# Performance work log

Measured on AMD Instinct MI355X. Metric: run time of the kernel, lower is better.

The kernel has to match this reference:

```python
import jax, jax.numpy as jnp
import numpy as np
from jax import lax

B_, L_, D_MODEL, D_FF = 8, 1024, 512, 2048
D_STATE, D_CONV, EXPAND = 16, 4, 2
D_IN = EXPAND * D_MODEL
DT_RANK = (D_MODEL + 15) // 16  # 32


def _ln(x, g, b, eps=1e-5):
    m = jnp.mean(x, -1, keepdims=True)
    v = jnp.var(x, -1, keepdims=True)
    return (x - m) / jnp.sqrt(v + eps) * g + b


def _selective_scan(u, dt, A, Bm, Cm, D):
    # u, dt: (B,L,d_in); Bm, Cm: (B,L,d_state); A: (d_in,d_state); D: (d_in,)
    def step(h, xs):
        dt_t, B_t, C_t, u_t = xs  # (B,d_in),(B,ds),(B,ds),(B,d_in)
        dA = jnp.exp(dt_t[..., None] * A)                       # (B,d_in,ds)
        h = dA * h + (dt_t * u_t)[..., None] * B_t[:, None, :]  # (B,d_in,ds)
        y = jnp.einsum('bds,bs->bd', h, C_t)
        return h, y

    h0 = jnp.zeros((u.shape[0], D_IN, D_STATE), u.dtype)
    xs = (dt.transpose(1, 0, 2), Bm.transpose(1, 0, 2),
          Cm.transpose(1, 0, 2), u.transpose(1, 0, 2))
    _, ys = lax.scan(step, h0, xs)           # (L,B,d_in)
    return ys.transpose(1, 0, 2) + u * D


def _mamba(x, in_w, conv_w, conv_b, xp_w, dtp_w, dtp_b, A_log, D, out_w):
    xz = x @ in_w.T                              # (B,L,2*d_in)
    xs, z = jnp.split(xz, 2, axis=-1)
    # causal depthwise conv1d over L
    xc = lax.conv_general_dilated(xs.transpose(0, 2, 1), conv_w, (1,),
                                  [(D_CONV - 1, 0)], feature_group_count=D_IN)
    xc = jax.nn.silu(xc + conv_b[None, :, None]).transpose(0, 2, 1)  # (B,L,d_in)
    x_dbl = xc @ xp_w.T
    dt, Bm, Cm = jnp.split(x_dbl, [DT_RANK, DT_RANK + D_STATE], axis=-1)
    dt = jax.nn.softplus(dt @ dtp_w.T + dtp_b)
    A = -jnp.exp(A_log)
    y = _selective_scan(xc, dt, A, Bm, Cm, D)
    y = y * jax.nn.silu(z)
    return y @ out_w.T


def _forward(x,
             in1_w, conv1d1_w, conv1d1_b, xp1_w, dtp1_w, dtp1_b, Alog1, D1, outp1_w,
             in2_w, conv1d2_w, conv1d2_b, xp2_w, dtp2_w, dtp2_b, Alog2, D2, outp2_w,
             c1_w, c1_b, c2_w, c2_b, ln1_g, ln1_b, ln2_g, ln2_b):
    x_res = x  # dropout is identity in eval
    fwd = _mamba(x, in1_w, conv1d1_w, conv1d1_b, xp1_w, dtp1_w, dtp1_b, Alog1, D1, outp1_w)
    bwd = _mamba(jnp.flip(x, 1), in2_w, conv1d2_w, conv1d2_b, xp2_w, dtp2_w, dtp2_b,
                 Alog2, D2, outp2_w)
    new_x = fwd + jnp.flip(bwd, 1)
    x = _ln(new_x + x_res, ln1_g, ln1_b)
    y = jax.nn.gelu(jnp.einsum('bld,fd->blf', x, c1_w[:, :, 0]) + c1_b, approximate=False)
    y = jnp.einsum('blf,df->bld', y, c2_w[:, :, 0]) + c2_b
    return _ln(x + y, ln2_g, ln2_b)


def setup_inputs() -> dict:
    key = jax.random.key(0)
    ks = iter(jax.random.split(key, 32))
    rn = lambda shape, s=0.02: jax.random.normal(next(ks), shape, jnp.float32) * s

    def mamba_params():
        return dict(in_w=rn((2 * D_IN, D_MODEL)), conv_w=rn((D_IN, 1, D_CONV)),
                    conv_b=rn((D_IN,)), xp_w=rn((DT_RANK + 2 * D_STATE, D_IN)),
                    dtp_w=rn((D_IN, DT_RANK)), dtp_b=rn((D_IN,)),
                    A_log=jnp.log(jnp.tile(jnp.arange(1., D_STATE + 1.), (D_IN, 1))).astype(jnp.float32),
                    D=jnp.ones((D_IN,), jnp.float32), out_w=rn((D_MODEL, D_IN)))

    m1, m2 = mamba_params(), mamba_params()
    return {
        'x': jax.random.normal(next(ks), (B_, L_, D_MODEL), jnp.float32),
        'in1_w': m1['in_w'], 'conv1d1_w': m1['conv_w'], 'conv1d1_b': m1['conv_b'],
        'xp1_w': m1['xp_w'], 'dtp1_w': m1['dtp_w'], 'dtp1_b': m1['dtp_b'],
        'Alog1': m1['A_log'], 'D1': m1['D'], 'outp1_w': m1['out_w'],
        'in2_w': m2['in_w'], 'conv1d2_w': m2['conv_w'], 'conv1d2_b': m2['conv_b'],
        'xp2_w': m2['xp_w'], 'dtp2_w': m2['dtp_w'], 'dtp2_b': m2['dtp_b'],
        'Alog2': m2['A_log'], 'D2': m2['D'], 'outp2_w': m2['out_w'],
        'c1_w': rn((D_FF, D_MODEL, 1)), 'c1_b': rn((D_FF,)),
        'c2_w': rn((D_MODEL, D_FF, 1)), 'c2_b': rn((D_MODEL,)),
        'ln1_g': jnp.ones((D_MODEL,), jnp.float32), 'ln1_b': jnp.zeros((D_MODEL,), jnp.float32),
        'ln2_g': jnp.ones((D_MODEL,), jnp.float32), 'ln2_b': jnp.zeros((D_MODEL,), jnp.float32),
    }


def reference(x,
              in1_w, conv1d1_w, conv1d1_b, xp1_w, dtp1_w, dtp1_b, Alog1, D1, outp1_w,
              in2_w, conv1d2_w, conv1d2_b, xp2_w, dtp2_w, dtp2_b, Alog2, D2, outp2_w,
              c1_w, c1_b, c2_w, c2_b, ln1_g, ln1_b, ln2_g, ln2_b):
    return _forward(x,
                    in1_w, conv1d1_w, conv1d1_b, xp1_w, dtp1_w, dtp1_b, Alog1, D1, outp1_w,
                    in2_w, conv1d2_w, conv1d2_b, xp2_w, dtp2_w, dtp2_b, Alog2, D2, outp2_w,
                    c1_w, c1_b, c2_w, c2_b, ln1_g, ln1_b, ln2_g, ln2_b)
```

## Files before the change

kernel.cpp:

```cpp
#include <hip/hip_runtime.h>
#include <hip/hip_bf16.h>
#include <math.h>

#define B_SZ 8
#define L_SZ 1024
#define DM 512
#define DFF 2048
#define DIN 1024
#define DSTATE 16
#define DTRANK 32
#define MROWS (B_SZ * L_SZ)
#define CH 256
#define NCH 4

typedef __hip_bfloat16 bf16;
typedef unsigned short u16;
using f32x4 = __attribute__((ext_vector_type(4))) float;
using bfrag = __attribute__((ext_vector_type(8))) short;

__device__ inline float ldf(const float* p, long i) { return p[i]; }
__device__ inline float ldf(const bf16* p, long i) {
  return __uint_as_float((unsigned)((const u16*)p)[i] << 16);
}
__device__ inline void stf(float* p, long i, float v) { p[i] = v; }
__device__ inline void stf(bf16* p, long i, float v) { p[i] = __float2bfloat16(v); }
__device__ inline float b2f(u16 x) {
  return __uint_as_float((unsigned)x << 16);
}
__device__ inline u16 f2b(float v) {
  union { bf16 h; u16 u; } c;
  c.h = __float2bfloat16(v);
  return c.u;
}

__device__ inline float fexp2(float x) {
  float r;
  asm("v_exp_f32 %0, %1" : "=v"(r) : "v"(x));
  return r;
}

typedef __attribute__((address_space(1))) const void g_void;
typedef __attribute__((address_space(3))) void l_void;
__device__ inline void gl_lds16(const void* g, void* l) {
  __builtin_amdgcn_global_load_lds((g_void*)g, (l_void*)l, 16, 0, 0);
}

__device__ inline float4 ld4f_bt(const float* p) { return *(const float4*)p; }
__device__ inline float4 ld4f_bt(const bf16* p) {
  ushort4 u = *(const ushort4*)p;
  float4 v;
  v.x = b2f(u.x); v.y = b2f(u.y); v.z = b2f(u.z); v.w = b2f(u.w);
  return v;
}

__device__ inline void ld16f(const float* p, uint4& lo, uint4& hi) {
  float4 a = *(const float4*)p, b = *(const float4*)(p + 4);
  float4 c = *(const float4*)(p + 8), d = *(const float4*)(p + 12);
  union { uint4 v; u16 s[8]; } L, H;
  L.s[0] = f2b(a.x); L.s[1] = f2b(a.y); L.s[2] = f2b(a.z); L.s[3] = f2b(a.w);
  L.s[4] = f2b(b.x); L.s[5] = f2b(b.y); L.s[6] = f2b(b.z); L.s[7] = f2b(b.w);
  H.s[0] = f2b(c.x); H.s[1] = f2b(c.y); H.s[2] = f2b(c.z); H.s[3] = f2b(c.w);
  H.s[4] = f2b(d.x); H.s[5] = f2b(d.y); H.s[6] = f2b(d.z); H.s[7] = f2b(d.w);
  lo = L.v; hi = H.v;
}

__device__ inline float dpp_add_r8(float x) {
  float r; asm("v_add_f32 %0, %1, %2 row_ror:8" : "=v"(r) : "v"(x), "v"(x)); return r;
}
__device__ inline float dpp_add_r4(float x) {
  float r; asm("v_add_f32 %0, %1, %2 row_ror:4" : "=v"(r) : "v"(x), "v"(x)); return r;
}
__device__ inline float dpp_add_r2(float x) {
  float r; asm("v_add_f32 %0, %1, %2 row_ror:2" : "=v"(r) : "v"(x), "v"(x)); return r;
}
__device__ inline float dpp_add_r1(float x) {
  float r; asm("v_add_f32 %0, %1, %2 row_ror:1" : "=v"(r) : "v"(x), "v"(x)); return r;
}
__device__ inline float row16_sum(float x) {
  return dpp_add_r1(dpp_add_r2(dpp_add_r4(dpp_add_r8(x))));
}

__device__ inline int flipL(int r) {
  int t = r & (L_SZ - 1);
  return (r - t) + (L_SZ - 1 - t);
}

__global__ __launch_bounds__(256) void cvt8_k(
    const float* s0, const float* s1, const float* s2, const float* s3,
    const float* s4, const float* s5, const float* s6, const float* s7,
    bf16* d0, bf16* d1, bf16* d2, bf16* d3,
    bf16* d4, bf16* d5, bf16* d6, bf16* d7) {
  int blk = blockIdx.x;
  const float* s; bf16* d; long off;
  if (blk < 2048)       { s = s0; d = d0; off = (long)blk * 256; }
  else if (blk < 4096)  { s = s1; d = d1; off = (long)(blk - 2048) * 256; }
  else if (blk < 6144)  { s = s2; d = d2; off = (long)(blk - 4096) * 256; }
  else if (blk < 8192)  { s = s3; d = d3; off = (long)(blk - 6144) * 256; }
  else if (blk < 10240) { s = s4; d = d4; off = (long)(blk - 8192) * 256; }
  else if (blk < 12288) { s = s5; d = d5; off = (long)(blk - 10240) * 256; }
  else if (blk < 16384) { s = s6; d = d6; off = (long)(blk - 12288) * 256; }
  else                  { s = s7; d = d7; off = (long)(blk - 16384) * 256; }
  off += threadIdx.x;
  d[off] = __float2bfloat16(s[off]);
}

constexpr int MEPI_STORE2 = 0;
constexpr int MEPI_GATE2 = 1;
constexpr int MEPI_BIAS_GELU = 2;
constexpr int MEPI_BIAS_RES = 3;

template <int EPI, typename TA, typename TO>
__global__ __launch_bounds__(256) void mgemm_k(
    const TA* __restrict__ Ab, int lda,
    const bf16* __restrict__ Wb, int ldw,
    TO* __restrict__ C, TO* __restrict__ C2, int ldc,
    const float* __restrict__ bias,
    const float* __restrict__ res,
    int K) {
  constexpr bool ABF = (sizeof(TA) == 2);
  __shared__ u16 Wsm[128][32];
  __shared__ u16 AsmL[ABF ? 128 : 1][32];
  __shared__ u16 AsmP[ABF ? 1 : 128][ABF ? 1 : 40];
  const int tid = threadIdx.x;
  const int m0 = blockIdx.y * 128;
  const int n0 = blockIdx.x * 128;

  const int srow4 = tid >> 2;
  const int q16 = tid & 3;
  const u16* Wg0 = (const u16*)Wb + (long)(n0 + srow4) * ldw + q16 * 8;
  const u16* Wg1 = (const u16*)Wb + (long)(n0 + 64 + srow4) * ldw + q16 * 8;
  char* WsmB = (char*)&Wsm[0][0] + (tid >> 6) * 1024;

  const u16* Ag0 = (const u16*)Ab + (long)(m0 + srow4) * lda + q16 * 8;
  const u16* Ag1 = (const u16*)Ab + (long)(m0 + 64 + srow4) * lda + q16 * 8;
  char* AsmB = (char*)&AsmL[0][0] + (tid >> 6) * 1024;

  const int srow = tid >> 1;
  const int scol = (tid & 1) * 16;
  const TA* Agf = Ab + (long)(m0 + srow) * lda + scol;

  const int lane = tid & 63, quad = lane >> 4, l16 = lane & 15;
  const int wid = tid >> 6;
  const int wm = (wid & 1) * 64, wn = (wid >> 1) * 64;

  f32x4 acc[4][4];
#pragma unroll
  for (int i = 0; i < 4; ++i)
#pragma unroll
    for (int j = 0; j < 4; ++j) acc[i][j] = {0.f, 0.f, 0.f, 0.f};

  for (int k0 = 0; k0 < K; k0 += 32) {
    uint4 av0, av1;
    if constexpr (!ABF) ld16f((const float*)(Agf + k0), av0, av1);
    __syncthreads();
    gl_lds16(Wg0 + k0, WsmB);
    gl_lds16(Wg1 + k0, WsmB + 4096);
    if constexpr (ABF) {
      gl_lds16(Ag0 + k0, AsmB);
      gl_lds16(Ag1 + k0, AsmB + 4096);
    } else {
      *(uint4*)&AsmP[srow][scol] = av0;
      *(uint4*)&AsmP[srow][scol + 8] = av1;
    }
    __syncthreads();
    bfrag a[4], b[4];
#pragma unroll
    for (int mi = 0; mi < 4; ++mi) {
      if constexpr (ABF)
        a[mi] = *(const bfrag*)&AsmL[wm + mi * 16 + l16][quad * 8];
      else
        a[mi] = *(const bfrag*)&AsmP[wm + mi * 16 + l16][quad * 8];
    }
#pragma unroll
    for (int ni = 0; ni < 4; ++ni)
      b[ni] = *(const bfrag*)&Wsm[wn + ni * 16 + l16][quad * 8];
#pragma unroll
    for (int mi = 0; mi < 4; ++mi)
#pragma unroll
      for (int ni = 0; ni < 4; ++ni)
        acc[mi][ni] = __builtin_amdgcn_mfma_f32_16x16x32_bf16(
            a[mi], b[ni], acc[mi][ni], 0, 0, 0);
  }

  const bool second = (n0 >= DIN);
#pragma unroll
  for (int mi = 0; mi < 4; ++mi)
#pragma unroll
    for (int ni = 0; ni < 4; ++ni)
#pragma unroll
      for (int r = 0; r < 4; ++r) {
        int row = m0 + wm + mi * 16 + quad * 4 + r;
        int col = n0 + wn + ni * 16 + l16;
        float v = acc[mi][ni][r];
        if (EPI == MEPI_STORE2) {
          if (second) stf(C2, (long)flipL(row) * ldc + (col - DIN), v);
          else stf(C, (long)row * ldc + col, v);
        } else if (EPI == MEPI_GATE2) {
          TO* T = second ? C2 : C;
          long oi = second ? ((long)flipL(row) * ldc + (col - DIN))
                           : ((long)row * ldc + col);
          float y = ldf((const bf16*)T, oi);
          float sz = v / (1.f + __expf(-v));
          stf(T, oi, y * sz);
        } else if (EPI == MEPI_BIAS_GELU) {
          long oi = (long)row * ldc + col;
          v += bias[col];
          v = 0.5f * v * (1.f + erff(v * 0.70710678118654752440f));
          stf(C, oi, v);
        } else if (EPI == MEPI_BIAS_RES) {
          long oi = (long)row * ldc + col;
          ((float*)C)[oi] = v + bias[col] + res[oi];
        }
      }
}

__global__ __launch_bounds__(256) void mmerge_k(
    const bf16* __restrict__ y1, const bf16* __restrict__ y2,
    const bf16* __restrict__ W1, const bf16* __restrict__ W2,
    const float* __restrict__ xres, float* __restrict__ newx) {
  __shared__ u16 AsmL[128][32];
  __shared__ u16 Wsm[128][32];
  const int tid = threadIdx.x;
  const int m0 = blockIdx.y * 128;
  const int n0 = blockIdx.x * 128;

  const int srow4 = tid >> 2;
  const int q16 = tid & 3;
  int r1a = m0 + srow4, r1b = m0 + 64 + srow4;
  int r2a = flipL(r1a), r2b = flipL(r1b);
  const u16* A1g0 = (const u16*)y1 + (long)r1a * DIN + q16 * 8;
  const u16* A1g1 = (const u16*)y1 + (long)r1b * DIN + q16 * 8;
  const u16* A2g0 = (const u16*)y2 + (long)r2a * DIN + q16 * 8;
  const u16* A2g1 = (const u16*)y2 + (long)r2b * DIN + q16 * 8;
  const u16* W1g0 = (const u16*)W1 + (long)(n0 + srow4) * DIN + q16 * 8;
  const u16* W1g1 = (const u16*)W1 + (long)(n0 + 64 + srow4) * DIN + q16 * 8;
  const u16* W2g0 = (const u16*)W2 + (long)(n0 + srow4) * DIN + q16 * 8;
  const u16* W2g1 = (const u16*)W2 + (long)(n0 + 64 + srow4) * DIN + q16 * 8;
  char* AsmB = (char*)&AsmL[0][0] + (tid >> 6) * 1024;
  char* WsmB = (char*)&Wsm[0][0] + (tid >> 6) * 1024;

  const int lane = tid & 63, quad = lane >> 4, l16 = lane & 15;
  const int wid = tid >> 6;
  const int wm = (wid & 1) * 64, wn = (wid >> 1) * 64;

  f32x4 acc[4][4];
#pragma unroll
  for (int i = 0; i < 4; ++i)
#pragma unroll
    for (int j = 0; j < 4; ++j) acc[i][j] = {0.f, 0.f, 0.f, 0.f};

  for (int k0 = 0; k0 < 2 * DIN; k0 += 32) {
    const bool ph2 = (k0 >= DIN);
    const int kk = k0 & (DIN - 1);
    const u16* a0 = ph2 ? A2g0 : A1g0;
    const u16* a1 = ph2 ? A2g1 : A1g1;
    const u16* w0 = ph2 ? W2g0 : W1g0;
    const u16* w1 = ph2 ? W2g1 : W1g1;
    __syncthreads();
    gl_lds16(a0 + kk, AsmB);
    gl_lds16(a1 + kk, AsmB + 4096);
    gl_lds16(w0 + kk, WsmB);
    gl_lds16(w1 + kk, WsmB + 4096);
    __syncthreads();
    bfrag a[4], b[4];
#pragma unroll
    for (int mi = 0; mi < 4; ++mi)
      a[mi] = *(const bfrag*)&AsmL[wm + mi * 16 + l16][quad * 8];
#pragma unroll
    for (int ni = 0; ni < 4; ++ni)
      b[ni] = *(const bfrag*)&Wsm[wn + ni * 16 + l16][quad * 8];
#pragma unroll
    for (int mi = 0; mi < 4; ++mi)
#pragma unroll
      for (int ni = 0; ni < 4; ++ni)
        acc[mi][ni] = __builtin_amdgcn_mfma_f32_16x16x32_bf16(
            a[mi], b[ni], acc[mi][ni], 0, 0, 0);
  }

#pragma unroll
  for (int mi = 0; mi < 4; ++mi)
#pragma unroll
    for (int ni = 0; ni < 4; ++ni)
#pragma unroll
      for (int r = 0; r < 4; ++r) {
        int row = m0 + wm + mi * 16 + quad * 4 + r;
        int col = n0 + wn + ni * 16 + l16;
        long oi = (long)row * DM + col;
        newx[oi] = acc[mi][ni][r] + xres[oi];
      }
}

constexpr int EPI_NONE = 0;
constexpr int EPI_SOFTPLUS_ROW = 1;

#define BM 64
#define BN 64
#define BKK 16

template <int EPI, typename TB, typename TO>
__global__ __launch_bounds__(256) void gemmBT_k(
    const float* __restrict__ A,
    const TB* __restrict__ B,
    TO* __restrict__ C, int N,
    const float* __restrict__ bias, int K) {
  __shared__ float As[BKK][BM + 4];
  __shared__ float Bs[BKK][BN + 4];
  const int tid = threadIdx.x;
  const int m0 = blockIdx.y * BM;
  const int n0 = blockIdx.x * BN;
  const int tx = tid & 15;
  const int ty = tid >> 4;
  const int lrow = tid >> 2;
  const int lcol = (tid & 3) * 4;
  const int kr = tid >> 4;
  const int nc = (tid & 15) * 4;

  const float* Arow = A + (long)(m0 + lrow) * K;

  float acc[4][4] = {};
  for (int k0 = 0; k0 < K; k0 += BKK) {
    float4 av = *(const float4*)(Arow + k0 + lcol);
    float4 bv = ld4f_bt(B + (long)(k0 + kr) * N + n0 + nc);
    As[lcol + 0][lrow] = av.x; As[lcol + 1][lrow] = av.y;
    As[lcol + 2][lrow] = av.z; As[lcol + 3][lrow] = av.w;
    Bs[kr][nc + 0] = bv.x; Bs[kr][nc + 1] = bv.y;
    Bs[kr][nc + 2] = bv.z; Bs[kr][nc + 3] = bv.w;
    __syncthreads();
#pragma unroll
    for (int k = 0; k < BKK; ++k) {
      float a[4], b[4];
#pragma unroll
      for (int i = 0; i < 4; ++i) a[i] = As[k][ty * 4 + i];
#pragma unroll
      for (int j = 0; j < 4; ++j) b[j] = Bs[k][tx * 4 + j];
#pragma unroll
      for (int i = 0; i < 4; ++i)
#pragma unroll
        for (int j = 0; j < 4; ++j) acc[i][j] += a[i] * b[j];
    }
    __syncthreads();
  }

#pragma unroll
  for (int i = 0; i < 4; ++i) {
    int r = m0 + ty * 4 + i;
#pragma unroll
    for (int j = 0; j < 4; ++j) {
      int c = n0 + tx * 4 + j;
      float v = acc[i][j];
      if (EPI == EPI_SOFTPLUS_ROW) {
        v += bias[r];
        v = (v > 20.f) ? v : log1pf(__expf(v));
      }
      stf(C, (long)r * N + c, v);
    }
  }
}

#define XSLICE 4
#define XSZ ((long)64 * MROWS)

__global__ __launch_bounds__(256) void xprojs_k(
    const float* __restrict__ A1, const bf16* __restrict__ B1,
    float* __restrict__ P1,
    const float* __restrict__ A2, const bf16* __restrict__ B2,
    float* __restrict__ P2) {
  __shared__ float As[BKK][BM + 4];
  __shared__ float Bs[BKK][BN + 4];
  const int tid = threadIdx.x;
  const int n0 = blockIdx.x * BN;
  const int slice = blockIdx.y;
  const int kbeg = slice * (DIN / XSLICE);
  const int dir = blockIdx.z;
  const float* A = dir ? A2 : A1;
  const bf16* Bm = dir ? B2 : B1;
  float* P = (dir ? P2 : P1) + (long)slice * XSZ;
  const int N = MROWS, K = DIN;
  const int tx = tid & 15;
  const int ty = tid >> 4;
  const int lrow = tid >> 2;
  const int lcol = (tid & 3) * 4;
  const int kr = tid >> 4;
  const int nc = (tid & 15) * 4;

  const float* Arow = A + (long)lrow * K;

  float acc[4][4] = {};
  for (int k0 = kbeg; k0 < kbeg + DIN / XSLICE; k0 += BKK) {
    float4 av = *(const float4*)(Arow + k0 + lcol);
    float4 bv = ld4f_bt(Bm + (long)(k0 + kr) * N + n0 + nc);
    As[lcol + 0][lrow] = av.x; As[lcol + 1][lrow] = av.y;
    As[lcol + 2][lrow] = av.z; As[lcol + 3][lrow] = av.w;
    Bs[kr][nc + 0] = bv.x; Bs[kr][nc + 1] = bv.y;
    Bs[kr][nc + 2] = bv.z; Bs[kr][nc + 3] = bv.w;
    __syncthreads();
#pragma unroll
    for (int k = 0; k < BKK; ++k) {
      float a[4], b[4];
#pragma unroll
      for (int i = 0; i < 4; ++i) a[i] = As[k][ty * 4 + i];
#pragma unroll
      for (int j = 0; j < 4; ++j) b[j] = Bs[k][tx * 4 + j];
#pragma unroll
      for (int i = 0; i < 4; ++i)
#pragma unroll
        for (int j = 0; j < 4; ++j) acc[i][j] += a[i] * b[j];
    }
    __syncthreads();
  }

#pragma unroll
  for (int i = 0; i < 4; ++i) {
    int r = ty * 4 + i;
#pragma unroll
    for (int j = 0; j < 4; ++j) {
      int c = n0 + tx * 4 + j;
      P[(long)r * N + c] = acc[i][j];
    }
  }
}

__global__ __launch_bounds__(256) void xred_k(
    const float* __restrict__ P1, float* __restrict__ o1,
    const float* __restrict__ P2, float* __restrict__ o2) {
  long i = (long)blockIdx.x * 256 + threadIdx.x;
  const float* P = blockIdx.y ? P2 : P1;
  float* o = blockIdx.y ? o2 : o1;
  o[i] = P[i] + P[i + XSZ] + P[i + 2 * XSZ] + P[i + 3 * XSZ];
}

__global__ __launch_bounds__(256) void convT_k(
    const bf16* __restrict__ xs, const float* __restrict__ w,
    const float* __restrict__ b, bf16* __restrict__ xcT) {
  __shared__ u16 T[64][72];
  int c0 = blockIdx.x * 64;
  int r0 = blockIdx.y * 64;
  int tid = threadIdx.x;
  int tr = tid >> 2;
  int tc = (tid & 3) * 16;

  const u16* src = (const u16*)xs + (long)(r0 + tr) * DIN + c0 + tc;
  uint4 v0 = *(const uint4*)src;
  uint4 v1 = *(const uint4*)(src + 8);
  u16 tmp[16];
  *(uint4*)tmp = v0;
  *(uint4*)(tmp + 8) = v1;
#pragma unroll
  for (int j = 0; j < 16; ++j) T[tc + j][tr + 3] = tmp[j];
  bool head = (r0 & (L_SZ - 1)) == 0;
  if (tid < 12) {
    int hr = tid >> 2;
    int seg = (tid & 3) * 16;
    if (head) {
#pragma unroll
      for (int j = 0; j < 16; ++j) T[seg + j][hr] = 0;
    } else {
      const u16* hs = (const u16*)xs + (long)(r0 - 3 + hr) * DIN + c0 + seg;
      uint4 h0 = *(const uint4*)hs;
      uint4 h1 = *(const uint4*)(hs + 8);
      u16 ht[16];
      *(uint4*)ht = h0;
      *(uint4*)(ht + 8) = h1;
#pragma unroll
      for (int j = 0; j < 16; ++j) T[seg + j][hr] = ht[j];
    }
  }
  __syncthreads();

  int d = c0 + tr;
  float w0 = w[d * 4 + 0], w1 = w[d * 4 + 1], w2 = w[d * 4 + 2], w3 = w[d * 4 + 3];
  float bd = b[d];
  float X[19];
#pragma unroll
  for (int k = 0; k < 19; ++k) X[k] = b2f(T[tr][tc + k]);
  u16 o[16];
#pragma unroll
  for (int j = 0; j < 16; ++j) {
    float acc = bd + w0 * X[j] + w1 * X[j + 1] + w2 * X[j + 2] + w3 * X[j + 3];
    o[j] = f2b(acc / (1.f + __expf(-acc)));
  }
  u16* dst = (u16*)xcT + (long)d * MROWS + r0 + tc;
  *(uint4*)dst = *(uint4*)o;
  *(uint4*)(dst + 8) = *(uint4*)(o + 8);
}

__global__ __launch_bounds__(256, 4) void scan1_k(
    const u16* __restrict__ dtT1, const u16* __restrict__ dtT2,
    const u16* __restrict__ uT1, const u16* __restrict__ uT2,
    const float* __restrict__ xd1, const float* __restrict__ xd2,
    const float* __restrict__ Alog1, const float* __restrict__ Alog2,
    bf16* __restrict__ hl1, bf16* __restrict__ hl2,
    float* __restrict__ sd1, float* __restrict__ sd2) {
  int blk = blockIdx.x;
  int dblk = blk & 15;
  int r = blk >> 4;
  int c = r % 3; r /= 3;
  int b = r & 7;
  int dir = r >> 3;
  int tid = threadIdx.x;
  int s = tid & 15;
  int gi = tid >> 4;
  int d0 = dblk * 64 + gi * 4;
  const u16* dtT = dir ? dtT2 : dtT1;
  const u16* uT = dir ? uT2 : uT1;
  const float* xd = dir ? xd2 : xd1;
  const float* Alog = dir ? Alog2 : Alog1;
  bf16* hl = dir ? hl2 : hl1;
  float* sd = dir ? sd2 : sd1;

  float A2[4], h[4], sdt[4];
#pragma unroll
  for (int dd = 0; dd < 4; ++dd) {
    A2[dd] = -__expf(Alog[(d0 + dd) * DSTATE + s]) * 1.4426950408889634f;
    h[dd] = 0.f;
    sdt[dd] = 0.f;
  }
  long t0 = (long)b * L_SZ + c * CH;
  const u16* pdt = dtT + (long)d0 * MROWS + t0;
  const u16* pu = uT + (long)d0 * MROWS + t0;
  const float* pB = xd + (long)(DTRANK + s) * MROWS + t0;

  for (int g = 0; g < CH / 8; ++g) {
    union { uint4 v; u16 a[8]; } dt8[4], u8[4];
    union { float4 v[2]; float a[8]; } B8;
#pragma unroll
    for (int dd = 0; dd < 4; ++dd) {
      dt8[dd].v = *(const uint4*)(pdt + (long)dd * MROWS + g * 8);
      u8[dd].v = *(const uint4*)(pu + (long)dd * MROWS + g * 8);
    }
    B8.v[0] = *(const float4*)(pB + g * 8);
    B8.v[1] = *(const float4*)(pB + g * 8 + 4);
#pragma unroll
    for (int j = 0; j < 8; ++j) {
      float Bj = B8.a[j];
#pragma unroll
      for (int dd = 0; dd < 4; ++dd) {
        float dtv = b2f(dt8[dd].a[j]);
        float uv = b2f(u8[dd].a[j]);
        float da = fexp2(dtv * A2[dd]);
        h[dd] = da * h[dd] + (dtv * uv) * Bj;
        sdt[dd] += dtv;
      }
    }
  }
#pragma unroll
  for (int dd = 0; dd < 4; ++dd) {
    int ci = (b * 3 + c) * 1024 + d0 + dd;
    hl[(long)ci * 16 + s] = __float2bfloat16(h[dd]);
    if (s == 0) sd[ci] = sdt[dd];
  }
}

__global__ __launch_bounds__(256, 4) void scan2_k(
    const u16* __restrict__ dtT1, const u16* __restrict__ dtT2,
    const u16* __restrict__ uT1, const u16* __restrict__ uT2,
    const float* __restrict__ xd1, const float* __restrict__ xd2,
    const float* __restrict__ Alog1, const float* __restrict__ Alog2,
    const float* __restrict__ D1, const float* __restrict__ D2,
    const bf16* __restrict__ hl1, const bf16* __restrict__ hl2,
    const float* __restrict__ sd1, const float* __restrict__ sd2,
    bf16* __restrict__ y1, bf16* __restrict__ y2) {
  int blk = blockIdx.x;
  int dblk = blk & 15;
  int c = (blk >> 4) & 3;
  int b = (blk >> 6) & 7;
  int dir = blk >> 9;
  int tid = threadIdx.x;
  int s = tid & 15;
  int gi = tid >> 4;
  int d0 = dblk * 64 + gi * 4;
  const u16* dtT = dir ? dtT2 : dtT1;
  const u16* uT = dir ? uT2 : uT1;
  const float* xd = dir ? xd2 : xd1;
  const float* Alog = dir ? Alog2 : Alog1;
  const float* Dp = dir ? D2 : D1;
  const bf16* hl = dir ? hl2 : hl1;
  const float* sd = dir ? sd2 : sd1;
  bf16* out = dir ? y2 : y1;

  float A2[4], h[4], Dd[4];
#pragma unroll
  for (int dd = 0; dd < 4; ++dd) {
    A2[dd] = -__expf(Alog[(d0 + dd) * DSTATE + s]) * 1.4426950408889634f;
    Dd[dd] = Dp[d0 + dd];
    h[dd] = 0.f;
  }

  for (int cc = 0; cc < c; ++cc) {
#pragma unroll
    for (int dd = 0; dd < 4; ++dd) {
      int ci = (b * 3 + cc) * 1024 + d0 + dd;
      float P = fexp2(A2[dd] * sd[ci]);
      h[dd] = h[dd] * P + b2f(((const u16*)hl)[(long)ci * 16 + s]);
    }
  }

  long t0 = (long)b * L_SZ + c * CH;
  const u16* pdt = dtT + (long)d0 * MROWS + t0;
  const u16* pu = uT + (long)d0 * MROWS + t0;
  const float* pB = xd + (long)(DTRANK + s) * MROWS + t0;
  const float* pC = xd + (long)(DTRANK + DSTATE + s) * MROWS + t0;
  u16* outb = (u16*)out + (long)b * L_SZ * DIN + (long)c * CH * DIN + d0;

  for (int g = 0; g < CH / 8; ++g) {
    union { uint4 v; u16 a[8]; } dt8[4], u8[4];
    union { float4 v[2]; float a[8]; } B8, C8;
#pragma unroll
    for (int dd = 0; dd < 4; ++dd) {
      dt8[dd].v = *(const uint4*)(pdt + (long)dd * MROWS + g * 8);
      u8[dd].v = *(const uint4*)(pu + (long)dd * MROWS + g * 8);
    }
    B8.v[0] = *(const float4*)(pB + g * 8);
    B8.v[1] = *(const float4*)(pB + g * 8 + 4);
    C8.v[0] = *(const float4*)(pC + g * 8);
    C8.v[1] = *(const float4*)(pC + g * 8 + 4);
    u16* og = outb + (long)g * 8 * DIN;
#pragma unroll
    for (int j = 0; j < 8; ++j) {
      float Bj = B8.a[j];
      float Cj = C8.a[j];
      u16 o4[4];
#pragma unroll
      for (int dd = 0; dd < 4; ++dd) {
        float dtv = b2f(dt8[dd].a[j]);
        float uv = b2f(u8[dd].a[j]);
        float da = fexp2(dtv * A2[dd]);
        h[dd] = da * h[dd] + (dtv * uv) * Bj;
        float q = row16_sum(h[dd] * Cj);
        o4[dd] = f2b(q + Dd[dd] * uv);
      }
      if (s == 0) *(uint2*)(og + (long)j * DIN) = *(uint2*)o4;
    }
  }
}

__global__ __launch_bounds__(256) void ln_k(
    const float* __restrict__ xin, const float* __restrict__ g,
    const float* __restrict__ bb, float* __restrict__ out,
    bf16* __restrict__ outb) {
  int row = blockIdx.x;
  const float* p = xin + (long)row * DM;
  int tid = threadIdx.x;
  float x0 = p[tid], x1 = p[tid + 256];
  float sum = x0 + x1;
  float sq = x0 * x0 + x1 * x1;
#pragma unroll
  for (int o = 1; o < 64; o <<= 1) {
    sum += __shfl_xor(sum, o, 64);
    sq += __shfl_xor(sq, o, 64);
  }
  __shared__ float ssum[4], ssq[4];
  int wv = tid >> 6;
  if ((tid & 63) == 0) { ssum[wv] = sum; ssq[wv] = sq; }
  __syncthreads();
  sum = ssum[0] + ssum[1] + ssum[2] + ssum[3];
  sq = ssq[0] + ssq[1] + ssq[2] + ssq[3];
  float mean = sum * (1.f / DM);
  float var = sq * (1.f / DM) - mean * mean;
  float rstd = rsqrtf(var + 1e-5f);
  float v0 = (x0 - mean) * rstd * g[tid] + bb[tid];
  float v1 = (x1 - mean) * rstd * g[tid + 256] + bb[tid + 256];
  out[(long)row * DM + tid] = v0;
  out[(long)row * DM + tid + 256] = v1;
  if (outb) {
    stf(outb, (long)row * DM + tid, v0);
    stf(outb, (long)row * DM + tid + 256, v1);
  }
}

extern "C" void kernel_launch(void* const* d_in, const int* in_sizes, int n_in,
                              void* d_out, int out_size, void* d_ws, size_t ws_size,
                              hipStream_t stream) {
  const float* x = (const float*)d_in[0];
  const float* in1_w = (const float*)d_in[1];
  const float* conv1_w = (const float*)d_in[2];
  const float* conv1_b = (const float*)d_in[3];
  const float* xp1_w = (const float*)d_in[4];
  const float* dtp1_w = (const float*)d_in[5];
  const float* dtp1_b = (const float*)d_in[6];
  const float* Alog1 = (const float*)d_in[7];
  const float* D1 = (const float*)d_in[8];
  const float* outp1_w = (const float*)d_in[9];
  const float* in2_w = (const float*)d_in[10];
  const float* conv2_w = (const float*)d_in[11];
  const float* conv2_b = (const float*)d_in[12];
  const float* xp2_w = (const float*)d_in[13];
  const float* dtp2_w = (const float*)d_in[14];
  const float* dtp2_b = (const float*)d_in[15];
  const float* Alog2 = (const float*)d_in[16];
  const float* D2 = (const float*)d_in[17];
  const float* outp2_w = (const float*)d_in[18];
  const float* c1_w = (const float*)d_in[19];
  const float* c1_b = (const float*)d_in[20];
  const float* c2_w = (const float*)d_in[21];
  const float* c2_b = (const float*)d_in[22];
  const float* ln1_g = (const float*)d_in[23];
  const float* ln1_b = (const float*)d_in[24];
  const float* ln2_g = (const float*)d_in[25];
  const float* ln2_b = (const float*)d_in[26];

  const long MB = 1024L * 1024;
  char* wsb = (char*)d_ws;
  bf16* A = (bf16*)(wsb + 0 * MB);
  bf16* B = (bf16*)(wsb + 16 * MB);
  bf16* C = (bf16*)(wsb + 32 * MB);
  bf16* D = (bf16*)(wsb + 48 * MB);
  bf16* E = (bf16*)(wsb + 64 * MB);
  bf16* F = (bf16*)(wsb + 80 * MB);
  float* Bf = (float*)B;
  float* Cf = (float*)C;
  float* Af = (float*)A;
  bf16* ffn = C;
  float* P1 = (float*)A;
  float* P2 = (float*)D;

  char* ob = (char*)d_out;
  bf16* Wxs = (bf16*)(ob + 0 * MB);
  bf16* Wg = (bf16*)(ob + 2 * MB);
  bf16* o1b = (bf16*)(ob + 4 * MB);
  bf16* o2b = (bf16*)(ob + 5 * MB);
  bf16* c1b = (bf16*)(ob + 6 * MB);
  bf16* c2b = (bf16*)(ob + 8 * MB);
  float* xdT1 = (float*)(ob + 10 * MB);
  float* xdT2 = (float*)(ob + 12 * MB);
  float* sd1 = (float*)(ob + 14 * MB);
  float* sd2 = (float*)(ob + 14 * MB + 131072);
  bf16* hl1 = (bf16*)(ob + 14 * MB + 262144);
  bf16* hl2 = (bf16*)(ob + 15 * MB);

  const long HWN = (long)DIN * DM;

  dim3 blk(256);
  dim3 gP2(2 * DIN / 128, MROWS / 128);
  dim3 gM(DM / 128, MROWS / 128);
  dim3 gF(DFF / 128, MROWS / 128);
  dim3 gC(DIN / 64, MROWS / 64);
  dim3 gXs(MROWS / BN, XSLICE, 2);
  dim3 gXr(XSZ / 256, 2);
  dim3 gD(MROWS / BN, DIN / BM);

  cvt8_k<<<20480, blk, 0, stream>>>(
      in1_w, in2_w, in1_w + HWN, in2_w + HWN, outp1_w, outp2_w, c1_w, c2_w,
      Wxs, Wxs + HWN, Wg, Wg + HWN, o1b, o2b, c1b, c2b);

  mgemm_k<MEPI_STORE2, float, bf16><<<gP2, blk, 0, stream>>>(
      x, DM, Wxs, DM, A, D, DIN, nullptr, nullptr, DM);

  convT_k<<<gC, blk, 0, stream>>>(A, conv1_w, conv1_b, B);
  convT_k<<<gC, blk, 0, stream>>>(D, conv2_w, conv2_b, E);

  xprojs_k<<<gXs, blk, 0, stream>>>(xp1_w, B, P1, xp2_w, E, P2);
  xred_k<<<gXr, blk, 0, stream>>>(P1, xdT1, P2, xdT2);

  gemmBT_k<EPI_SOFTPLUS_ROW, float, bf16><<<gD, blk, 0, stream>>>(
      dtp1_w, xdT1, C, MROWS, dtp1_b, DTRANK);
  gemmBT_k<EPI_SOFTPLUS_ROW, float, bf16><<<gD, blk, 0, stream>>>(
      dtp2_w, xdT2, F, MROWS, dtp2_b, DTRANK);

  scan1_k<<<2 * 8 * 3 * 16, blk, 0, stream>>>(
      (const u16*)C, (const u16*)F, (const u16*)B, (const u16*)E,
      xdT1, xdT2, Alog1, Alog2, hl1, hl2, sd1, sd2);
  scan2_k<<<2 * 8 * 4 * 16, blk, 0, stream>>>(
      (const u16*)C, (const u16*)F, (const u16*)B, (const u16*)E,
      xdT1, xdT2, Alog1, Alog2, D1, D2, hl1, hl2, sd1, sd2, A, D);

  mgemm_k<MEPI_GATE2, float, bf16><<<gP2, blk, 0, stream>>>(
      x, DM, Wg, DM, A, D, DIN, nullptr, nullptr, DM);

  mmerge_k<<<gM, blk, 0, stream>>>(A, D, o1b, o2b, x, Cf);

  ln_k<<<MROWS, blk, 0, stream>>>(Cf, ln1_g, ln1_b, Bf, E);

  mgemm_k<MEPI_BIAS_GELU, bf16, bf16><<<gF, blk, 0, stream>>>(
      E, DM, c1b, DM, ffn, nullptr, DFF, c1_b, nullptr, DM);
  mgemm_k<MEPI_BIAS_RES, bf16, float><<<gM, blk, 0, stream>>>(
      ffn, DFF, c2b, DFF, Af, nullptr, DM, c2_b, Bf, DFF);

  ln_k<<<MROWS, blk, 0, stream>>>(Af, ln2_g, ln2_b, (float*)d_out, nullptr);
}
```

Before: 726.5 us.

## Pre-convert x to bf16, shrink N=512 GEMM tiles, batch both directions per launch

Converts the fp32 input x to bf16 up front, adding it to the weight-conversion kernel and a separate conversion before the gate GEMM, so the in-projection GEMMs can stream A via global_load_lds instead of converting on load. The out-projection merge and FFN second GEMM (N=512) switch from 128x128 tiles to 64x64 tiles, giving more blocks on the GPU for these narrow outputs. The conv and dt-projection kernels now handle both directions in one launch via blockIdx.z. These changes add extra conversion passes over x and smaller tiles with less reuse per block, in exchange for fewer launches and better occupancy.

After: 765.0 us. 5.3% more time.

```diff
diff --git a/kernel.cpp b/kernel.cpp
--- a/kernel.cpp
+++ b/kernel.cpp
@@ -53,17 +53,6 @@
   return v;
 }
 
-__device__ inline void ld16f(const float* p, uint4& lo, uint4& hi) {
-  float4 a = *(const float4*)p, b = *(const float4*)(p + 4);
-  float4 c = *(const float4*)(p + 8), d = *(const float4*)(p + 12);
-  union { uint4 v; u16 s[8]; } L, H;
-  L.s[0] = f2b(a.x); L.s[1] = f2b(a.y); L.s[2] = f2b(a.z); L.s[3] = f2b(a.w);
-  L.s[4] = f2b(b.x); L.s[5] = f2b(b.y); L.s[6] = f2b(b.z); L.s[7] = f2b(b.w);
-  H.s[0] = f2b(c.x); H.s[1] = f2b(c.y); H.s[2] = f2b(c.z); H.s[3] = f2b(c.w);
-  H.s[4] = f2b(d.x); H.s[5] = f2b(d.y); H.s[6] = f2b(d.z); H.s[7] = f2b(d.w);
-  lo = L.v; hi = H.v;
-}
-
 __device__ inline float dpp_add_r8(float x) {
   float r; asm("v_add_f32 %0, %1, %2 row_ror:8" : "=v"(r) : "v"(x), "v"(x)); return r;
 }
@@ -85,11 +74,18 @@
   return (r - t) + (L_SZ - 1 - t);
 }
 
-__global__ __launch_bounds__(256) void cvt8_k(
+__global__ __launch_bounds__(256) void cvt_k(const float* __restrict__ s,
+                                             bf16* __restrict__ d, int n) {
+  int i = blockIdx.x * 256 + threadIdx.x;
+  if (i < n) d[i] = __float2bfloat16(s[i]);
+}
+
+__global__ __launch_bounds__(256) void cvt9_k(
     const float* s0, const float* s1, const float* s2, const float* s3,
     const float* s4, const float* s5, const float* s6, const float* s7,
+    const float* s8,
     bf16* d0, bf16* d1, bf16* d2, bf16* d3,
-    bf16* d4, bf16* d5, bf16* d6, bf16* d7) {
+    bf16* d4, bf16* d5, bf16* d6, bf16* d7, bf16* d8) {
   int blk = blockIdx.x;
   const float* s; bf16* d; long off;
   if (blk < 2048)       { s = s0; d = d0; off = (long)blk * 256; }
@@ -99,7 +95,8 @@
   else if (blk < 10240) { s = s4; d = d4; off = (long)(blk - 8192) * 256; }
   else if (blk < 12288) { s = s5; d = d5; off = (long)(blk - 10240) * 256; }
   else if (blk < 16384) { s = s6; d = d6; off = (long)(blk - 12288) * 256; }
-  else                  { s = s7; d = d7; off = (long)(blk - 16384) * 256; }
+  else if (blk < 20480) { s = s7; d = d7; off = (long)(blk - 16384) * 256; }
+  else                  { s = s8; d = d8; off = (long)(blk - 20480) * 256; }
   off += threadIdx.x;
   d[off] = __float2bfloat16(s[off]);
 }
@@ -107,20 +104,16 @@
 constexpr int MEPI_STORE2 = 0;
 constexpr int MEPI_GATE2 = 1;
 constexpr int MEPI_BIAS_GELU = 2;
-constexpr int MEPI_BIAS_RES = 3;
-
-template <int EPI, typename TA, typename TO>
+
+template <int EPI, typename TO>
 __global__ __launch_bounds__(256) void mgemm_k(
-    const TA* __restrict__ Ab, int lda,
+    const bf16* __restrict__ Ab, int lda,
     const bf16* __restrict__ Wb, int ldw,
     TO* __restrict__ C, TO* __restrict__ C2, int ldc,
     const float* __restrict__ bias,
-    const float* __restrict__ res,
     int K) {
-  constexpr bool ABF = (sizeof(TA) == 2);
   __shared__ u16 Wsm[128][32];
-  __shared__ u16 AsmL[ABF ? 128 : 1][32];
-  __shared__ u16 AsmP[ABF ? 1 : 128][ABF ? 1 : 40];
+  __shared__ u16 AsmL[128][32];
   const int tid = threadIdx.x;
   const int m0 = blockIdx.y * 128;
   const int n0 = blockIdx.x * 128;
@@ -135,10 +128,6 @@
   const u16* Ag1 = (const u16*)Ab + (long)(m0 + 64 + srow4) * lda + q16 * 8;
   char* AsmB = (char*)&AsmL[0][0] + (tid >> 6) * 1024;
 
-  const int srow = tid >> 1;
-  const int scol = (tid & 1) * 16;
-  const TA* Agf = Ab + (long)(m0 + srow) * lda + scol;
-
   const int lane = tid & 63, quad = lane >> 4, l16 = lane & 15;
   const int wid = tid >> 6;
   const int wm = (wid & 1) * 64, wn = (wid >> 1) * 64;
@@ -150,27 +139,16 @@
     for (int j = 0; j < 4; ++j) acc[i][j] = {0.f, 0.f, 0.f, 0.f};
 
   for (int k0 = 0; k0 < K; k0 += 32) {
-    uint4 av0, av1;
-    if constexpr (!ABF) ld16f((const float*)(Agf + k0), av0, av1);
     __syncthreads();
     gl_lds16(Wg0 + k0, WsmB);
     gl_lds16(Wg1 + k0, WsmB + 4096);
-    if constexpr (ABF) {
-      gl_lds16(Ag0 + k0, AsmB);
-      gl_lds16(Ag1 + k0, AsmB + 4096);
-    } else {
-      *(uint4*)&AsmP[srow][scol] = av0;
-      *(uint4*)&AsmP[srow][scol + 8] = av1;
-    }
+    gl_lds16(Ag0 + k0, AsmB);
+    gl_lds16(Ag1 + k0, AsmB + 4096);
     __syncthreads();
     bfrag a[4], b[4];
 #pragma unroll
-    for (int mi = 0; mi < 4; ++mi) {
-      if constexpr (ABF)
-        a[mi] = *(const bfrag*)&AsmL[wm + mi * 16 + l16][quad * 8];
-      else
-        a[mi] = *(const bfrag*)&AsmP[wm + mi * 16 + l16][quad * 8];
-    }
+    for (int mi = 0; mi < 4; ++mi)
+      a[mi] = *(const bfrag*)&AsmL[wm + mi * 16 + l16][quad * 8];
 #pragma unroll
     for (int ni = 0; ni < 4; ++ni)
       b[ni] = *(const bfrag*)&Wsm[wn + ni * 16 + l16][quad * 8];
@@ -207,107 +185,136 @@
           v += bias[col];
           v = 0.5f * v * (1.f + erff(v * 0.70710678118654752440f));
           stf(C, oi, v);
-        } else if (EPI == MEPI_BIAS_RES) {
-          long oi = (long)row * ldc + col;
-          ((float*)C)[oi] = v + bias[col] + res[oi];
         }
       }
 }
 
-__global__ __launch_bounds__(256) void mmerge_k(
+__global__ __launch_bounds__(256) void mmerge64_k(
     const bf16* __restrict__ y1, const bf16* __restrict__ y2,
     const bf16* __restrict__ W1, const bf16* __restrict__ W2,
     const float* __restrict__ xres, float* __restrict__ newx) {
-  __shared__ u16 AsmL[128][32];
-  __shared__ u16 Wsm[128][32];
+  __shared__ u16 Asm[64][32];
+  __shared__ u16 Wsm[64][32];
   const int tid = threadIdx.x;
-  const int m0 = blockIdx.y * 128;
-  const int n0 = blockIdx.x * 128;
+  const int m0 = blockIdx.y * 64;
+  const int n0 = blockIdx.x * 64;
 
   const int srow4 = tid >> 2;
   const int q16 = tid & 3;
-  int r1a = m0 + srow4, r1b = m0 + 64 + srow4;
-  int r2a = flipL(r1a), r2b = flipL(r1b);
-  const u16* A1g0 = (const u16*)y1 + (long)r1a * DIN + q16 * 8;
-  const u16* A1g1 = (const u16*)y1 + (long)r1b * DIN + q16 * 8;
-  const u16* A2g0 = (const u16*)y2 + (long)r2a * DIN + q16 * 8;
-  const u16* A2g1 = (const u16*)y2 + (long)r2b * DIN + q16 * 8;
-  const u16* W1g0 = (const u16*)W1 + (long)(n0 + srow4) * DIN + q16 * 8;
-  const u16* W1g1 = (const u16*)W1 + (long)(n0 + 64 + srow4) * DIN + q16 * 8;
-  const u16* W2g0 = (const u16*)W2 + (long)(n0 + srow4) * DIN + q16 * 8;
-  const u16* W2g1 = (const u16*)W2 + (long)(n0 + 64 + srow4) * DIN + q16 * 8;
-  char* AsmB = (char*)&AsmL[0][0] + (tid >> 6) * 1024;
+  const u16* A1g = (const u16*)y1 + (long)(m0 + srow4) * DIN + q16 * 8;
+  const u16* A2g = (const u16*)y2 + (long)flipL(m0 + srow4) * DIN + q16 * 8;
+  const u16* W1g = (const u16*)W1 + (long)(n0 + srow4) * DIN + q16 * 8;
+  const u16* W2g = (const u16*)W2 + (long)(n0 + srow4) * DIN + q16 * 8;
+  char* AsmB = (char*)&Asm[0][0] + (tid >> 6) * 1024;
   char* WsmB = (char*)&Wsm[0][0] + (tid >> 6) * 1024;
 
-  const int lane = tid & 63, quad = lane >> 4, l16 = lane & 15;
-  const int wid = tid >> 6;
-  const int wm = (wid & 1) * 64, wn = (wid >> 1) * 64;
-
-  f32x4 acc[4][4];
-#pragma unroll
-  for (int i = 0; i < 4; ++i)
-#pragma unroll
-    for (int j = 0; j < 4; ++j) acc[i][j] = {0.f, 0.f, 0.f, 0.f};
+  const int w = tid >> 6, lane = tid & 63, quad = lane >> 4, l16 = lane & 15;
+
+  f32x4 acc[4];
+#pragma unroll
+  for (int j = 0; j < 4; ++j) acc[j] = {0.f, 0.f, 0.f, 0.f};
 
   for (int k0 = 0; k0 < 2 * DIN; k0 += 32) {
     const bool ph2 = (k0 >= DIN);
     const int kk = k0 & (DIN - 1);
-    const u16* a0 = ph2 ? A2g0 : A1g0;
-    const u16* a1 = ph2 ? A2g1 : A1g1;
-    const u16* w0 = ph2 ? W2g0 : W1g0;
-    const u16* w1 = ph2 ? W2g1 : W1g1;
-    __syncthreads();
-    gl_lds16(a0 + kk, AsmB);
-    gl_lds16(a1 + kk, AsmB + 4096);
-    gl_lds16(w0 + kk, WsmB);
-    gl_lds16(w1 + kk, WsmB + 4096);
-    __syncthreads();
-    bfrag a[4], b[4];
-#pragma unroll
-    for (int mi = 0; mi < 4; ++mi)
-      a[mi] = *(const bfrag*)&AsmL[wm + mi * 16 + l16][quad * 8];
+    const u16* asrc = ph2 ? A2g : A1g;
+    const u16* wsrc = ph2 ? W2g : W1g;
+    __syncthreads();
+    gl_lds16(asrc + kk, AsmB);
+    gl_lds16(wsrc + kk, WsmB);
+    __syncthreads();
+    bfrag a = *(const bfrag*)&Asm[w * 16 + l16][quad * 8];
+    bfrag b[4];
 #pragma unroll
     for (int ni = 0; ni < 4; ++ni)
-      b[ni] = *(const bfrag*)&Wsm[wn + ni * 16 + l16][quad * 8];
-#pragma unroll
-    for (int mi = 0; mi < 4; ++mi)
-#pragma unroll
-      for (int ni = 0; ni < 4; ++ni)
-        acc[mi][ni] = __builtin_amdgcn_mfma_f32_16x16x32_bf16(
-            a[mi], b[ni], acc[mi][ni], 0, 0, 0);
-  }
-
-#pragma unroll
-  for (int mi = 0; mi < 4; ++mi)
+      b[ni] = *(const bfrag*)&Wsm[ni * 16 + l16][quad * 8];
 #pragma unroll
     for (int ni = 0; ni < 4; ++ni)
-#pragma unroll
-      for (int r = 0; r < 4; ++r) {
-        int row = m0 + wm + mi * 16 + quad * 4 + r;
-        int col = n0 + wn + ni * 16 + l16;
-        long oi = (long)row * DM + col;
-        newx[oi] = acc[mi][ni][r] + xres[oi];
-      }
-}
-
-constexpr int EPI_NONE = 0;
-constexpr int EPI_SOFTPLUS_ROW = 1;
+      acc[ni] = __builtin_amdgcn_mfma_f32_16x16x32_bf16(a, b[ni], acc[ni], 0, 0, 0);
+  }
+
+#pragma unroll
+  for (int ni = 0; ni < 4; ++ni)
+#pragma unroll
+    for (int r = 0; r < 4; ++r) {
+      int row = m0 + w * 16 + quad * 4 + r;
+      int col = n0 + ni * 16 + l16;
+      long oi = (long)row * DM + col;
+      newx[oi] = acc[ni][r] + xres[oi];
+    }
+}
+
+__global__ __launch_bounds__(256) void gemm64_br_k(
+    const bf16* __restrict__ Ab, int lda,
+    const bf16* __restrict__ Wb, int ldw,
+    float* __restrict__ Cout, int ldc,
+    const float* __restrict__ bias,
+    const float* __restrict__ res, int K) {
+  __shared__ u16 Asm[64][32];
+  __shared__ u16 Wsm[64][32];
+  const int tid = threadIdx.x;
+  const int m0 = blockIdx.y * 64;
+  const int n0 = blockIdx.x * 64;
+
+  const int srow4 = tid >> 2;
+  const int q16 = tid & 3;
+  const u16* Ag = (const u16*)Ab + (long)(m0 + srow4) * lda + q16 * 8;
+  const u16* Wg = (const u16*)Wb + (long)(n0 + srow4) * ldw + q16 * 8;
+  char* AsmB = (char*)&Asm[0][0] + (tid >> 6) * 1024;
+  char* WsmB = (char*)&Wsm[0][0] + (tid >> 6) * 1024;
+
+  const int w = tid >> 6, lane = tid & 63, quad = lane >> 4, l16 = lane & 15;
+
+  f32x4 acc[4];
+#pragma unroll
+  for (int j = 0; j < 4; ++j) acc[j] = {0.f, 0.f, 0.f, 0.f};
+
+  for (int k0 = 0; k0 < K; k0 += 32) {
+    __syncthreads();
+    gl_lds16(Ag + k0, AsmB);
+    gl_lds16(Wg + k0, WsmB);
+    __syncthreads();
+    bfrag a = *(const bfrag*)&Asm[w * 16 + l16][quad * 8];
+    bfrag b[4];
+#pragma unroll
+    for (int ni = 0; ni < 4; ++ni)
+      b[ni] = *(const bfrag*)&Wsm[ni * 16 + l16][quad * 8];
+#pragma unroll
+    for (int ni = 0; ni < 4; ++ni)
+      acc[ni] = __builtin_amdgcn_mfma_f32_16x16x32_bf16(a, b[ni], acc[ni], 0, 0, 0);
+  }
+
+#pragma unroll
+  for (int ni = 0; ni < 4; ++ni)
+#pragma unroll
+    for (int r = 0; r < 4; ++r) {
+      int row = m0 + w * 16 + quad * 4 + r;
+      int col = n0 + ni * 16 + l16;
+      long oi = (long)row * ldc + col;
+      Cout[oi] = acc[ni][r] + bias[col] + res[oi];
+    }
+}
 
 #define BM 64
 #define BN 64
 #define BKK 16
 
-template <int EPI, typename TB, typename TO>
-__global__ __launch_bounds__(256) void gemmBT_k(
-    const float* __restrict__ A,
-    const TB* __restrict__ B,
-    TO* __restrict__ C, int N,
-    const float* __restrict__ bias, int K) {
+__global__ __launch_bounds__(256) void dtT2_k(
+    const float* __restrict__ A1, const float* __restrict__ A2,
+    const float* __restrict__ B1, const float* __restrict__ B2,
+    bf16* __restrict__ C1, bf16* __restrict__ C2,
+    const float* __restrict__ bias1, const float* __restrict__ bias2) {
   __shared__ float As[BKK][BM + 4];
   __shared__ float Bs[BKK][BN + 4];
   const int tid = threadIdx.x;
   const int m0 = blockIdx.y * BM;
   const int n0 = blockIdx.x * BN;
+  const int dir = blockIdx.z;
+  const float* A = dir ? A2 : A1;
+  const float* B = dir ? B2 : B1;
+  bf16* C = dir ? C2 : C1;
+  const float* bias = dir ? bias2 : bias1;
+  const int N = MROWS, K = DTRANK;
   const int tx = tid & 15;
   const int ty = tid >> 4;
   const int lrow = tid >> 2;
@@ -320,7 +327,7 @@
   float acc[4][4] = {};
   for (int k0 = 0; k0 < K; k0 += BKK) {
     float4 av = *(const float4*)(Arow + k0 + lcol);
-    float4 bv = ld4f_bt(B + (long)(k0 + kr) * N + n0 + nc);
+    float4 bv = *(const float4*)(B + (long)(k0 + kr) * N + n0 + nc);
     As[lcol + 0][lrow] = av.x; As[lcol + 1][lrow] = av.y;
     As[lcol + 2][lrow] = av.z; As[lcol + 3][lrow] = av.w;
     Bs[kr][nc + 0] = bv.x; Bs[kr][nc + 1] = bv.y;
@@ -344,14 +351,12 @@
 #pragma unroll
   for (int i = 0; i < 4; ++i) {
     int r = m0 + ty * 4 + i;
+    float bs = bias[r];
 #pragma unroll
     for (int j = 0; j < 4; ++j) {
       int c = n0 + tx * 4 + j;
-      float v = acc[i][j];
-      if (EPI == EPI_SOFTPLUS_ROW) {
-        v += bias[r];
-        v = (v > 20.f) ? v : log1pf(__expf(v));
-      }
+      float v = acc[i][j] + bs;
+      v = (v > 20.f) ? v : log1pf(__expf(v));
       stf(C, (long)r * N + c, v);
     }
   }
@@ -429,12 +434,19 @@
   o[i] = P[i] + P[i + XSZ] + P[i + 2 * XSZ] + P[i + 3 * XSZ];
 }
 
-__global__ __launch_bounds__(256) void convT_k(
-    const bf16* __restrict__ xs, const float* __restrict__ w,
-    const float* __restrict__ b, bf16* __restrict__ xcT) {
+__global__ __launch_bounds__(256) void convT2_k(
+    const bf16* __restrict__ xs1, const bf16* __restrict__ xs2,
+    const float* __restrict__ w1, const float* __restrict__ w2,
+    const float* __restrict__ b1, const float* __restrict__ b2,
+    bf16* __restrict__ o1, bf16* __restrict__ o2) {
   __shared__ u16 T[64][72];
   int c0 = blockIdx.x * 64;
   int r0 = blockIdx.y * 64;
+  int dir = blockIdx.z;
+  const bf16* xs = dir ? xs2 : xs1;
+  const float* w = dir ? w2 : w1;
+  const float* b = dir ? b2 : b1;
+  bf16* xcT = dir ? o2 : o1;
   int tid = threadIdx.x;
   int tr = tid >> 2;
   int tc = (tid & 3) * 16;
@@ -468,7 +480,7 @@
   __syncthreads();
 
   int d = c0 + tr;
-  float w0 = w[d * 4 + 0], w1 = w[d * 4 + 1], w2 = w[d * 4 + 2], w3 = w[d * 4 + 3];
+  float w0 = w[d * 4 + 0], wq1 = w[d * 4 + 1], wq2 = w[d * 4 + 2], wq3 = w[d * 4 + 3];
   float bd = b[d];
   float X[19];
 #pragma unroll
@@ -476,7 +488,7 @@
   u16 o[16];
 #pragma unroll
   for (int j = 0; j < 16; ++j) {
-    float acc = bd + w0 * X[j] + w1 * X[j + 1] + w2 * X[j + 2] + w3 * X[j + 3];
+    float acc = bd + w0 * X[j] + wq1 * X[j + 1] + wq2 * X[j + 2] + wq3 * X[j + 3];
     o[j] = f2b(acc / (1.f + __expf(-acc)));
   }
   u16* dst = (u16*)xcT + (long)d * MROWS + r0 + tc;
@@ -713,6 +725,8 @@
   bf16* ffn = C;
   float* P1 = (float*)A;
   float* P2 = (float*)D;
+  bf16* xb = B;
+  bf16* xb2 = F;
 
   char* ob = (char*)d_out;
   bf16* Wxs = (bf16*)(ob + 0 * MB);
@@ -732,30 +746,28 @@
 
   dim3 blk(256);
   dim3 gP2(2 * DIN / 128, MROWS / 128);
-  dim3 gM(DM / 128, MROWS / 128);
+  dim3 gM64(DM / 64, MROWS / 64);
   dim3 gF(DFF / 128, MROWS / 128);
-  dim3 gC(DIN / 64, MROWS / 64);
+  dim3 gC2(DIN / 64, MROWS / 64, 2);
   dim3 gXs(MROWS / BN, XSLICE, 2);
   dim3 gXr(XSZ / 256, 2);
-  dim3 gD(MROWS / BN, DIN / BM);
-
-  cvt8_k<<<20480, blk, 0, stream>>>(
-      in1_w, in2_w, in1_w + HWN, in2_w + HWN, outp1_w, outp2_w, c1_w, c2_w,
-      Wxs, Wxs + HWN, Wg, Wg + HWN, o1b, o2b, c1b, c2b);
-
-  mgemm_k<MEPI_STORE2, float, bf16><<<gP2, blk, 0, stream>>>(
-      x, DM, Wxs, DM, A, D, DIN, nullptr, nullptr, DM);
-
-  convT_k<<<gC, blk, 0, stream>>>(A, conv1_w, conv1_b, B);
-  convT_k<<<gC, blk, 0, stream>>>(D, conv2_w, conv2_b, E);
+  dim3 gD2(MROWS / BN, DIN / BM, 2);
+
+  cvt9_k<<<36864, blk, 0, stream>>>(
+      in1_w, in2_w, in1_w + HWN, in2_w + HWN, outp1_w, outp2_w, c1_w, c2_w, x,
+      Wxs, Wxs + HWN, Wg, Wg + HWN, o1b, o2b, c1b, c2b, xb);
+
+  mgemm_k<MEPI_STORE2, bf16><<<gP2, blk, 0, stream>>>(
+      xb, DM, Wxs, DM, A, D, DIN, nullptr, DM);
+
+  convT2_k<<<gC2, blk, 0, stream>>>(A, D, conv1_w, conv2_w, conv1_b, conv2_b,
+                                    B, E);
 
   xprojs_k<<<gXs, blk, 0, stream>>>(xp1_w, B, P1, xp2_w, E, P2);
   xred_k<<<gXr, blk, 0, stream>>>(P1, xdT1, P2, xdT2);
 
-  gemmBT_k<EPI_SOFTPLUS_ROW, float, bf16><<<gD, blk, 0, stream>>>(
-      dtp1_w, xdT1, C, MROWS, dtp1_b, DTRANK);
-  gemmBT_k<EPI_SOFTPLUS_ROW, float, bf16><<<gD, blk, 0, stream>>>(
-      dtp2_w, xdT2, F, MROWS, dtp2_b, DTRANK);
+  dtT2_k<<<gD2, blk, 0, stream>>>(dtp1_w, dtp2_w, xdT1, xdT2, C, F,
+                                  dtp1_b, dtp2_b);
 
   scan1_k<<<2 * 8 * 3 * 16, blk, 0, stream>>>(
       (const u16*)C, (const u16*)F, (const u16*)B, (const u16*)E,
@@ -764,17 +776,18 @@
       (const u16*)C, (const u16*)F, (const u16*)B, (const u16*)E,
       xdT1, xdT2, Alog1, Alog2, D1, D2, hl1, hl2, sd1, sd2, A, D);
 
-  mgemm_k<MEPI_GATE2, float, bf16><<<gP2, blk, 0, stream>>>(
-      x, DM, Wg, DM, A, D, DIN, nullptr, nullptr, DM);
-
-  mmerge_k<<<gM, blk, 0, stream>>>(A, D, o1b, o2b, x, Cf);
+  cvt_k<<<(MROWS * DM) / 256, blk, 0, stream>>>(x, xb2, MROWS * DM);
+  mgemm_k<MEPI_GATE2, bf16><<<gP2, blk, 0, stream>>>(
+      xb2, DM, Wg, DM, A, D, DIN, nullptr, DM);
+
+  mmerge64_k<<<gM64, blk, 0, stream>>>(A, D, o1b, o2b, x, Cf);
 
   ln_k<<<MROWS, blk, 0, stream>>>(Cf, ln1_g, ln1_b, Bf, E);
 
-  mgemm_k<MEPI_BIAS_GELU, bf16, bf16><<<gF, blk, 0, stream>>>(
-      E, DM, c1b, DM, ffn, nullptr, DFF, c1_b, nullptr, DM);
-  mgemm_k<MEPI_BIAS_RES, bf16, float><<<gM, blk, 0, stream>>>(
-      ffn, DFF, c2b, DFF, Af, nullptr, DM, c2_b, Bf, DFF);
+  mgemm_k<MEPI_BIAS_GELU, bf16><<<gF, blk, 0, stream>>>(
+      E, DM, c1b, DM, ffn, nullptr, DFF, c1_b, DM);
+  gemm64_br_k<<<gM64, blk, 0, stream>>>(
+      ffn, DFF, c2b, DFF, Af, DM, c2_b, Bf, DFF);
 
   ln_k<<<MROWS, blk, 0, stream>>>(Af, ln2_g, ln2_b, (float*)d_out, nullptr);
 }
```
